# Kernel tuning notes

Hardware: AMD Instinct MI355X
Metric: run time of the kernel (lower is better)

## Reference

```python
import jax, jax.numpy as jnp
import numpy as np

BN_EPS = 1e-5


def setup_inputs() -> dict:
    key = jax.random.key(0)
    ks = jax.random.split(key, 8)
    B, C, N = 4, 256, 4096
    s = 1.0 / np.sqrt(C)
    return {
        "feature": jax.random.normal(ks[0], (B, C, N, 1), dtype=jnp.float32),
        "Wa": jax.random.normal(ks[1], (C, C), dtype=jnp.float32) * s,
        "ba": jnp.zeros((C,), dtype=jnp.float32),
        "Wb": jax.random.normal(ks[2], (C, C), dtype=jnp.float32) * s,
        "bb": jnp.zeros((C,), dtype=jnp.float32),
        "Wm": jax.random.normal(ks[3], (C, C), dtype=jnp.float32) * s,
        "bm": jnp.zeros((C,), dtype=jnp.float32),
        "gamma": jnp.ones((C,), dtype=jnp.float32),
        "beta": jnp.zeros((C,), dtype=jnp.float32),
        "rmean": jnp.zeros((C,), dtype=jnp.float32),
        "rvar": jnp.ones((C,), dtype=jnp.float32),
        "alpha": jnp.zeros((1,), dtype=jnp.float32),
    }


def reference(feature, Wa, ba, Wb, bb, Wm, bm, gamma, beta, rmean, rvar, alpha):
    # feature: [B, C, N, 1]; 1x1 convs are per-point linear maps over channels.
    x = feature[..., 0]  # [B, C, N]
    a = jnp.einsum('oc,bcn->bon', Wa, x) + ba[None, :, None]  # fc_a
    b = jnp.einsum('oc,bcn->bon', Wb, x) + bb[None, :, None]  # fc_b
    # att = softmax(a^T @ b) over last dim: [B, N, N]
    att = jax.nn.softmax(jnp.einsum('bcn,bcm->bnm', a, b), axis=2)
    # mlp: 1x1 conv + eval-mode BatchNorm
    m = jnp.einsum('oc,bcn->bon', Wm, x) + bm[None, :, None]
    inv = jax.lax.rsqrt(rvar + BN_EPS)
    m = (m - rmean[None, :, None]) * (inv * gamma)[None, :, None] + beta[None, :, None]
    # f = att @ m^T -> [B, N, C], back to [B, C, N]
    f = jnp.einsum('bnm,bcm->bcn', att, m)
    return feature + alpha[0] * f[..., None]
```

## Files before the change

### kernel.cpp

```cpp
#include <hip/hip_runtime.h>
#include <hip/hip_bf16.h>

typedef __bf16 bf16x8 __attribute__((ext_vector_type(8)));
typedef float f32x4 __attribute__((ext_vector_type(4)));
typedef float f32x16 __attribute__((ext_vector_type(16)));
typedef int i32x2 __attribute__((ext_vector_type(2)));
typedef int i32x4 __attribute__((ext_vector_type(4)));
typedef int i32x8 __attribute__((ext_vector_type(8)));
typedef unsigned int u32;

#define MFMA16 __builtin_amdgcn_mfma_f32_16x16x32_bf16
#define MFMASC(a, b, c) \
  __builtin_amdgcn_mfma_scale_f32_32x32x64_f8f6f4((a), (b), (c), 0, 0, 0, 0x7F7F7F7F, 0, 0x7F7F7F7F)

#define LOG2E 1.44269504f

__device__ __forceinline__ unsigned short f2b(float f) {
  return __builtin_bit_cast(unsigned short, (__bf16)f);
}

__device__ __forceinline__ u32 pk4(float a, float b, float c, float d) {
  int v = __builtin_amdgcn_cvt_pk_fp8_f32(a, b, 0, false);
  v = __builtin_amdgcn_cvt_pk_fp8_f32(c, d, v, true);
  return (u32)v;
}

__device__ __forceinline__ void gload_lds16(const void* g, void* l) {
  __builtin_amdgcn_global_load_lds(
      (const __attribute__((address_space(1))) unsigned int*)g,
      (__attribute__((address_space(3))) unsigned int*)l, 16, 0, 0);
}

__global__ __launch_bounds__(256) void k_wconv(const float* __restrict__ Wa,
                                               const float* __restrict__ Wb,
                                               const float* __restrict__ Wm,
                                               unsigned short* __restrict__ W16) {
  const int m = blockIdx.y;
  const float* W = (m == 0) ? Wa : (m == 1) ? Wb : Wm;
  const int i = (blockIdx.x * 256 + threadIdx.x) * 8;
  float4 a = *reinterpret_cast<const float4*>(W + i);
  float4 b = *reinterpret_cast<const float4*>(W + i + 4);
  ushort4 lo, hi;
  lo.x = f2b(a.x); lo.y = f2b(a.y); lo.z = f2b(a.z); lo.w = f2b(a.w);
  hi.x = f2b(b.x); hi.y = f2b(b.y); hi.z = f2b(b.z); hi.w = f2b(b.w);
  unsigned short* dst = W16 + m * 65536 + i;
  *reinterpret_cast<ushort4*>(dst) = lo;
  *reinterpret_cast<ushort4*>(dst + 4) = hi;
}

__global__ __launch_bounds__(256) void k_proj(
    const float* __restrict__ x, const unsigned short* __restrict__ W16,
    const float* __restrict__ ba, const float* __restrict__ bb,
    const float* __restrict__ bm, const float* __restrict__ gamma,
    const float* __restrict__ beta, const float* __restrict__ rmean,
    const float* __restrict__ rvar,
    unsigned char* __restrict__ Q8, unsigned char* __restrict__ K8,
    unsigned char* __restrict__ V8) {
  __shared__ float tile[256][33];
  __shared__ __align__(16) unsigned short XT_lds[32 * 256];
  const int nt = blockIdx.x, b = blockIdx.y;
  const int n0 = nt * 32;
  const int tid = threadIdx.x, w = tid >> 6, l = tid & 63;
  const int li = l & 15, lk = l >> 4;
  {
    const int cr = tid >> 3, j4 = (tid & 7) * 4;
#pragma unroll
    for (int p = 0; p < 8; ++p) {
      int c = p * 32 + cr;
      float4 v = *reinterpret_cast<const float4*>(
          x + ((size_t)(b * 256 + c)) * 4096 + n0 + j4);
      tile[c][j4] = v.x; tile[c][j4 + 1] = v.y;
      tile[c][j4 + 2] = v.z; tile[c][j4 + 3] = v.w;
    }
  }
  __syncthreads();
  {
    const int n = tid & 31, cb8 = (tid >> 5) * 32;
#pragma unroll
    for (int p = 0; p < 8; ++p) {
      int c0 = cb8 + p * 4;
      ushort4 o;
      o.x = f2b(tile[c0][n]); o.y = f2b(tile[c0 + 1][n]);
      o.z = f2b(tile[c0 + 2][n]); o.w = f2b(tile[c0 + 3][n]);
      unsigned off = ((unsigned)(n * 512 + c0 * 2)) ^ (unsigned)((n & 7) << 4);
      *reinterpret_cast<ushort4*>((char*)XT_lds + off) = o;
    }
  }
  __syncthreads();
  bf16x8 af[2][8];
#pragma unroll
  for (int rs = 0; rs < 2; ++rs) {
    const int row = rs * 16 + li;
#pragma unroll
    for (int kk = 0; kk < 8; ++kk) {
      unsigned off = ((unsigned)(row * 512 + kk * 64 + lk * 16)) ^ (unsigned)((row & 7) << 4);
      af[rs][kk] = *reinterpret_cast<const bf16x8*>((const char*)XT_lds + off);
    }
  }
  const int ofb = w * 4;
  f32x4 zero = {0.f, 0.f, 0.f, 0.f};
  f32x4 acc[2][4];
  {
#pragma unroll
    for (int rs = 0; rs < 2; ++rs)
#pragma unroll
      for (int i = 0; i < 4; ++i) acc[rs][i] = zero;
#pragma unroll
    for (int kk = 0; kk < 8; ++kk)
#pragma unroll
      for (int of = 0; of < 4; ++of) {
        bf16x8 bfv = *reinterpret_cast<const bf16x8*>(
            W16 + (size_t)((ofb + of) * 16 + li) * 256 + kk * 32 + lk * 8);
        acc[0][of] = MFMA16(bfv, af[0][kk], acc[0][of], 0, 0, 0);
        acc[1][of] = MFMA16(bfv, af[1][kk], acc[1][of], 0, 0, 0);
      }
#pragma unroll
    for (int rs = 0; rs < 2; ++rs) {
      const int n = n0 + rs * 16 + li;
      unsigned char* out = Q8 + ((size_t)b * 4096 + n) * 256;
#pragma unroll
      for (int of = 0; of < 4; ++of) {
        int c0 = (ofb + of) * 16 + lk * 4;
        float4 bs = *reinterpret_cast<const float4*>(ba + c0);
        u32 v = pk4((acc[rs][of][0] + bs.x) * LOG2E, (acc[rs][of][1] + bs.y) * LOG2E,
                    (acc[rs][of][2] + bs.z) * LOG2E, (acc[rs][of][3] + bs.w) * LOG2E);
        *reinterpret_cast<u32*>(out + c0) = v;
      }
    }
  }
  {
#pragma unroll
    for (int rs = 0; rs < 2; ++rs)
#pragma unroll
      for (int i = 0; i < 4; ++i) acc[rs][i] = zero;
#pragma unroll
    for (int kk = 0; kk < 8; ++kk)
#pragma unroll
      for (int of = 0; of < 4; ++of) {
        bf16x8 bfv = *reinterpret_cast<const bf16x8*>(
            W16 + 65536 + (size_t)((ofb + of) * 16 + li) * 256 + kk * 32 + lk * 8);
        acc[0][of] = MFMA16(bfv, af[0][kk], acc[0][of], 0, 0, 0);
        acc[1][of] = MFMA16(bfv, af[1][kk], acc[1][of], 0, 0, 0);
      }
#pragma unroll
    for (int rs = 0; rs < 2; ++rs) {
      const int n = n0 + rs * 16 + li;
      unsigned char* out = K8 + ((size_t)b * 4096 + n) * 256;
#pragma unroll
      for (int of = 0; of < 4; ++of) {
        int c0 = (ofb + of) * 16 + lk * 4;
        float4 bs = *reinterpret_cast<const float4*>(bb + c0);
        u32 v = pk4(acc[rs][of][0] + bs.x, acc[rs][of][1] + bs.y,
                    acc[rs][of][2] + bs.z, acc[rs][of][3] + bs.w);
        *reinterpret_cast<u32*>(out + c0) = v;
      }
    }
  }
  {
#pragma unroll
    for (int rs = 0; rs < 2; ++rs)
#pragma unroll
      for (int i = 0; i < 4; ++i) acc[rs][i] = zero;
#pragma unroll
    for (int kk = 0; kk < 8; ++kk)
#pragma unroll
      for (int of = 0; of < 4; ++of) {
        bf16x8 bfv = *reinterpret_cast<const bf16x8*>(
            W16 + 131072 + (size_t)((ofb + of) * 16 + li) * 256 + kk * 32 + lk * 8);
        acc[0][of] = MFMA16(af[0][kk], bfv, acc[0][of], 0, 0, 0);
        acc[1][of] = MFMA16(af[1][kk], bfv, acc[1][of], 0, 0, 0);
      }
#pragma unroll
    for (int of = 0; of < 4; ++of) {
      int c = (ofb + of) * 16 + li;
      float g = rsqrtf(rvar[c] + 1e-5f) * gamma[c];
      float sh = (bm[c] - rmean[c]) * g + beta[c];
#pragma unroll
      for (int rs = 0; rs < 2; ++rs) {
        const int nn0 = n0 + rs * 16 + lk * 4;
        u32 v = pk4(acc[rs][of][0] * g + sh, acc[rs][of][1] * g + sh,
                    acc[rs][of][2] * g + sh, acc[rs][of][3] * g + sh);
        *reinterpret_cast<u32*>(V8 + (((size_t)b * 512 + (nn0 >> 3)) * 256 + c) * 8 + (nn0 & 7)) = v;
      }
    }
  }
}

__global__ __launch_bounds__(256, 2) void k_attn(
    const unsigned char* __restrict__ Q8, const unsigned char* __restrict__ K8,
    const unsigned char* __restrict__ V8, unsigned short* __restrict__ part,
    float* __restrict__ mpart, float* __restrict__ lpart) {
  __shared__ __align__(16) unsigned char K_lds[2][64 * 256];
  __shared__ __align__(16) unsigned char V_lds[2][8 * 2048];
  const int bid = blockIdx.x;
  const int swz = (bid & 7) * 64 + (bid >> 3);
  const int qt = swz & 31;
  const int bs = swz >> 5;
  const int b = bs >> 2, s = bs & 3;
  const int tid = threadIdx.x, w = tid >> 6, l = tid & 63;
  const int q = l & 31, hi = l >> 5;
  const int rowq = qt * 128 + w * 32 + q;
  i32x8 qf8[4];
  const unsigned char* qp = Q8 + ((size_t)b * 4096 + rowq) * 256 + hi * 32;
#pragma unroll
  for (int kk = 0; kk < 4; ++kk) {
    i32x4 lo = *reinterpret_cast<const i32x4*>(qp + kk * 64);
    i32x4 hh = *reinterpret_cast<const i32x4*>(qp + kk * 64 + 16);
    qf8[kk] = (i32x8){lo[0], lo[1], lo[2], lo[3], hh[0], hh[1], hh[2], hh[3]};
  }
  f32x16 acc[8];
#pragma unroll
  for (int i = 0; i < 8; ++i)
#pragma unroll
    for (int r = 0; r < 16; ++r) acc[i][r] = 0.f;
  float mr = -3e38f, lr = 0.f;

  auto stageK = [&](int buf, int k0) {
#pragma unroll
    for (int g = 0; g < 4; ++g) {
      int row = w * 16 + g * 4 + (l >> 4);
      int c16 = (l & 15) ^ ((row & 7) << 1);
      const unsigned char* src = K8 + ((size_t)b * 4096 + k0 + row) * 256 + c16 * 16;
      gload_lds16(src, &K_lds[buf][(w * 16 + g * 4) * 256]);
    }
  };
  auto stageV = [&](int buf, int k0) {
    const size_t k8b = (size_t)b * 512 + (k0 >> 3);
#pragma unroll
    for (int g = 0; g < 4; ++g) {
      int slab = w * 2 + (g >> 1);
      int pos = (g & 1) * 64 + l;
      const unsigned char* src = V8 + (k8b + slab) * 2048 + pos * 16;
      gload_lds16(src, &V_lds[buf][slab * 2048 + (g & 1) * 1024]);
    }
  };

  const int kbase = s * 1024;
  stageK(0, kbase);
  stageV(0, kbase);
  asm volatile("s_waitcnt vmcnt(0)" ::: "memory");
  __syncthreads();
  int cur = 0;
  for (int t = 0; t < 16; ++t) {
    if (t < 15) { stageK(cur ^ 1, kbase + (t + 1) * 64); stageV(cur ^ 1, kbase + (t + 1) * 64); }
    f32x16 S0, S1;
#pragma unroll
    for (int r = 0; r < 16; ++r) { S0[r] = 0.f; S1[r] = 0.f; }
    __builtin_amdgcn_s_setprio(1);
#pragma unroll
    for (int kk = 0; kk < 4; ++kk) {
      int off = ((kk * 2 + hi) ^ (q & 7)) << 5;
      const unsigned char* kr0 = &K_lds[cur][q * 256 + off];
      const unsigned char* kr1 = &K_lds[cur][(32 + q) * 256 + off];
      i32x4 a0 = *reinterpret_cast<const i32x4*>(kr0);
      i32x4 a1 = *reinterpret_cast<const i32x4*>(kr0 + 16);
      i32x4 b0 = *reinterpret_cast<const i32x4*>(kr1);
      i32x4 b1 = *reinterpret_cast<const i32x4*>(kr1 + 16);
      i32x8 kf0 = (i32x8){a0[0], a0[1], a0[2], a0[3], a1[0], a1[1], a1[2], a1[3]};
      i32x8 kf1 = (i32x8){b0[0], b0[1], b0[2], b0[3], b1[0], b1[1], b1[2], b1[3]};
      S0 = MFMASC(kf0, qf8[kk], S0);
      S1 = MFMASC(kf1, qf8[kk], S1);
    }
    __builtin_amdgcn_s_setprio(0);
    float pmax = fmaxf(S0[0], S1[0]);
#pragma unroll
    for (int r = 1; r < 16; ++r) pmax = fmaxf(pmax, fmaxf(S0[r], S1[r]));
    pmax = fmaxf(pmax, __shfl_xor(pmax, 32));
    if (!__all(pmax - mr <= 7.0f)) {
      float nm = fmaxf(mr, pmax);
      float sc = exp2f(mr - nm);
      mr = nm;
      lr *= sc;
#pragma unroll
      for (int cb = 0; cb < 8; ++cb)
#pragma unroll
        for (int r = 0; r < 16; ++r) acc[cb][r] *= sc;
    }
    float p0[16], p1[16];
    float sum = 0.f;
#pragma unroll
    for (int r = 0; r < 16; ++r) { p0[r] = exp2f(S0[r] - mr); sum += p0[r]; }
#pragma unroll
    for (int r = 0; r < 16; ++r) { p1[r] = exp2f(S1[r] - mr); sum += p1[r]; }
    sum += __shfl_xor(sum, 32);
    lr += sum;
    u32 A0 = pk4(p0[0], p0[1], p0[2], p0[3]);
    u32 A1 = pk4(p0[4], p0[5], p0[6], p0[7]);
    u32 A2 = pk4(p0[8], p0[9], p0[10], p0[11]);
    u32 A3 = pk4(p0[12], p0[13], p0[14], p0[15]);
    u32 B0 = pk4(p1[0], p1[1], p1[2], p1[3]);
    u32 B1 = pk4(p1[4], p1[5], p1[6], p1[7]);
    u32 B2 = pk4(p1[8], p1[9], p1[10], p1[11]);
    u32 B3 = pk4(p1[12], p1[13], p1[14], p1[15]);
    asm volatile("v_permlane32_swap_b32 %0, %1" : "+v"(A0), "+v"(B0));
    asm volatile("v_permlane32_swap_b32 %0, %1" : "+v"(A1), "+v"(B1));
    asm volatile("v_permlane32_swap_b32 %0, %1" : "+v"(A2), "+v"(B2));
    asm volatile("v_permlane32_swap_b32 %0, %1" : "+v"(A3), "+v"(B3));
    i32x8 pb = (i32x8){(int)A0, (int)B0, (int)A1, (int)B1,
                       (int)A2, (int)B2, (int)A3, (int)B3};
    __builtin_amdgcn_s_setprio(1);
#pragma unroll
    for (int cb = 0; cb < 8; ++cb) {
      const unsigned char* vb = &V_lds[cur][(hi * 4) * 2048 + (cb * 32 + q) * 8];
      i32x2 v0 = *reinterpret_cast<const i32x2*>(vb);
      i32x2 v1 = *reinterpret_cast<const i32x2*>(vb + 2048);
      i32x2 v2 = *reinterpret_cast<const i32x2*>(vb + 4096);
      i32x2 v3 = *reinterpret_cast<const i32x2*>(vb + 6144);
      i32x8 vf = (i32x8){v0[0], v0[1], v1[0], v1[1], v2[0], v2[1], v3[0], v3[1]};
      acc[cb] = MFMASC(vf, pb, acc[cb]);
    }
    __builtin_amdgcn_s_setprio(0);
    asm volatile("s_waitcnt vmcnt(0)" ::: "memory");
    __syncthreads();
    cur ^= 1;
  }
  const int sb = s * 4 + b;
  size_t pbase = ((size_t)sb * 4096 + rowq) * 256;
#pragma unroll
  for (int cb = 0; cb < 8; ++cb)
#pragma unroll
    for (int g = 0; g < 4; ++g) {
      ushort4 o;
      o.x = f2b(acc[cb][g * 4 + 0]); o.y = f2b(acc[cb][g * 4 + 1]);
      o.z = f2b(acc[cb][g * 4 + 2]); o.w = f2b(acc[cb][g * 4 + 3]);
      *reinterpret_cast<ushort4*>(&part[pbase + cb * 32 + g * 8 + hi * 4]) = o;
    }
  if (hi == 0) {
    mpart[sb * 4096 + rowq] = mr;
    lpart[sb * 4096 + rowq] = lr;
  }
}

__global__ __launch_bounds__(256) void k_comb(
    const unsigned short* __restrict__ part, const float* __restrict__ mpart,
    const float* __restrict__ lpart, const float* __restrict__ feat,
    const float* __restrict__ alpha, float* __restrict__ out) {
  __shared__ float wgt[4][64];
  __shared__ float tile[64][261];
  const int nt = blockIdx.x, b = blockIdx.y;
  const int n0 = nt * 64;
  const int tid = threadIdx.x;
  if (tid < 64) {
    int qn = n0 + tid;
    float m[4], lv[4];
#pragma unroll
    for (int s = 0; s < 4; ++s) {
      m[s] = mpart[(s * 4 + b) * 4096 + qn];
      lv[s] = lpart[(s * 4 + b) * 4096 + qn];
    }
    float M = fmaxf(fmaxf(m[0], m[1]), fmaxf(m[2], m[3]));
    float e[4], L = 0.f;
#pragma unroll
    for (int s = 0; s < 4; ++s) { e[s] = exp2f(m[s] - M); L += e[s] * lv[s]; }
    float inv = 1.0f / L;
#pragma unroll
    for (int s = 0; s < 4; ++s) wgt[s][tid] = e[s] * inv;
  }
  __syncthreads();
  const int row = tid >> 2;
  const int c0 = (tid & 3) * 64;
  float acc[64];
#pragma unroll
  for (int k = 0; k < 64; ++k) acc[k] = 0.f;
  for (int s = 0; s < 4; ++s) {
    float ww = wgt[s][row];
    const unsigned short* p = part + (((size_t)(s * 4 + b)) * 4096 + n0 + row) * 256 + c0;
#pragma unroll
    for (int ch = 0; ch < 8; ++ch) {
      bf16x8 v = *reinterpret_cast<const bf16x8*>(p + ch * 8);
#pragma unroll
      for (int j = 0; j < 8; ++j) acc[ch * 8 + j] += ww * (float)v[j];
    }
  }
#pragma unroll
  for (int k = 0; k < 64; ++k) tile[row][c0 + k] = acc[k];
  __syncthreads();
  const float av = alpha[0];
  const int j = tid & 15, cb = tid >> 4;
#pragma unroll
  for (int p = 0; p < 16; ++p) {
    int c = cb * 16 + p;
    size_t gbase = ((size_t)(b * 256 + c)) * 4096 + n0 + j * 4;
    float4 f4 = *reinterpret_cast<const float4*>(feat + gbase);
    float4 o;
    o.x = f4.x + av * tile[j * 4 + 0][c];
    o.y = f4.y + av * tile[j * 4 + 1][c];
    o.z = f4.z + av * tile[j * 4 + 2][c];
    o.w = f4.w + av * tile[j * 4 + 3][c];
    *reinterpret_cast<float4*>(out + gbase) = o;
  }
}

extern "C" void kernel_launch(void* const* d_in, const int* in_sizes, int n_in,
                              void* d_out, int out_size, void* d_ws, size_t ws_size,
                              hipStream_t stream) {
  const float* feat  = (const float*)d_in[0];
  const float* Wa    = (const float*)d_in[1];
  const float* ba    = (const float*)d_in[2];
  const float* Wb    = (const float*)d_in[3];
  const float* bb    = (const float*)d_in[4];
  const float* Wm    = (const float*)d_in[5];
  const float* bm    = (const float*)d_in[6];
  const float* gamma = (const float*)d_in[7];
  const float* beta  = (const float*)d_in[8];
  const float* rmean = (const float*)d_in[9];
  const float* rvar  = (const float*)d_in[10];
  const float* alpha = (const float*)d_in[11];
  float* out = (float*)d_out;
  char* ws = (char*)d_ws;
  unsigned char*  Q8   = (unsigned char*)(ws);
  unsigned char*  K8   = (unsigned char*)(ws + ((size_t)4 << 20));
  unsigned char*  V8   = (unsigned char*)(ws + ((size_t)8 << 20));
  unsigned short* part = (unsigned short*)(ws + ((size_t)16 << 20));
  unsigned short* W16  = (unsigned short*)(ws + ((size_t)48 << 20));
  float* mpart = (float*)(ws + ((size_t)48 << 20) + 393216);
  float* lpart = (float*)(ws + ((size_t)48 << 20) + 393216 + 262144);

  k_wconv<<<dim3(32, 3), 256, 0, stream>>>(Wa, Wb, Wm, W16);
  k_proj<<<dim3(128, 4), 256, 0, stream>>>(feat, W16, ba, bb, bm, gamma, beta,
                                           rmean, rvar, Q8, K8, V8);
  k_attn<<<dim3(512), 256, 0, stream>>>(Q8, K8, V8, part, mpart, lpart);
  k_comb<<<dim3(64, 4), 256, 0, stream>>>(part, mpart, lpart, feat, alpha, out);
}
```

Baseline: 121.2 us.

## Re-layout V8 into 32-key chunks for wide LDS reads and unroll attn loop

Changes the V8 global layout from 8-key slabs to 32-key chunks per channel so each lane reads a contiguous 32-byte fragment from LDS instead of four 8-byte pieces. K fragment reads also become single 32-byte loads. Staging pointers are precomputed and the double-buffered loop is unrolled by two so buffer indices are compile-time constants. The max and sum reductions become trees, and the projection tile store becomes one float4 with padding changed to 36. Padding 36 may add bank conflicts in the transposed column reads, and 32-byte V reads with a 32-byte row stride could conflict in LDS.

```diff
diff --git a/kernel.cpp b/kernel.cpp
--- a/kernel.cpp
+++ b/kernel.cpp
@@ -4,7 +4,6 @@
 typedef __bf16 bf16x8 __attribute__((ext_vector_type(8)));
 typedef float f32x4 __attribute__((ext_vector_type(4)));
 typedef float f32x16 __attribute__((ext_vector_type(16)));
-typedef int i32x2 __attribute__((ext_vector_type(2)));
 typedef int i32x4 __attribute__((ext_vector_type(4)));
 typedef int i32x8 __attribute__((ext_vector_type(8)));
 typedef unsigned int u32;
@@ -56,7 +55,7 @@
     const float* __restrict__ rvar,
     unsigned char* __restrict__ Q8, unsigned char* __restrict__ K8,
     unsigned char* __restrict__ V8) {
-  __shared__ float tile[256][33];
+  __shared__ float tile[256][36];
   __shared__ __align__(16) unsigned short XT_lds[32 * 256];
   const int nt = blockIdx.x, b = blockIdx.y;
   const int n0 = nt * 32;
@@ -69,8 +68,7 @@
       int c = p * 32 + cr;
       float4 v = *reinterpret_cast<const float4*>(
           x + ((size_t)(b * 256 + c)) * 4096 + n0 + j4);
-      tile[c][j4] = v.x; tile[c][j4 + 1] = v.y;
-      tile[c][j4 + 2] = v.z; tile[c][j4 + 3] = v.w;
+      *reinterpret_cast<float4*>(&tile[c][j4]) = v;
     }
   }
   __syncthreads();
@@ -180,7 +178,8 @@
         const int nn0 = n0 + rs * 16 + lk * 4;
         u32 v = pk4(acc[rs][of][0] * g + sh, acc[rs][of][1] * g + sh,
                     acc[rs][of][2] * g + sh, acc[rs][of][3] * g + sh);
-        *reinterpret_cast<u32*>(V8 + (((size_t)b * 512 + (nn0 >> 3)) * 256 + c) * 8 + (nn0 & 7)) = v;
+        *reinterpret_cast<u32*>(
+            V8 + ((size_t)b * 128 + (nn0 >> 5)) * 8192 + c * 32 + (nn0 & 31)) = v;
       }
     }
   }
@@ -190,8 +189,8 @@
     const unsigned char* __restrict__ Q8, const unsigned char* __restrict__ K8,
     const unsigned char* __restrict__ V8, unsigned short* __restrict__ part,
     float* __restrict__ mpart, float* __restrict__ lpart) {
-  __shared__ __align__(16) unsigned char K_lds[2][64 * 256];
-  __shared__ __align__(16) unsigned char V_lds[2][8 * 2048];
+  __shared__ __align__(32) unsigned char K_lds[2][64 * 256];
+  __shared__ __align__(32) unsigned char V_lds[2][2 * 8192];
   const int bid = blockIdx.x;
   const int swz = (bid & 7) * 64 + (bid >> 3);
   const int qt = swz & 31;
@@ -215,57 +214,51 @@
     for (int r = 0; r < 16; ++r) acc[i][r] = 0.f;
   float mr = -3e38f, lr = 0.f;
 
-  auto stageK = [&](int buf, int k0) {
-#pragma unroll
-    for (int g = 0; g < 4; ++g) {
-      int row = w * 16 + g * 4 + (l >> 4);
-      int c16 = (l & 15) ^ ((row & 7) << 1);
-      const unsigned char* src = K8 + ((size_t)b * 4096 + k0 + row) * 256 + c16 * 16;
-      gload_lds16(src, &K_lds[buf][(w * 16 + g * 4) * 256]);
-    }
+  const int kbase = s * 1024;
+  const unsigned char* kp[4];
+  const unsigned char* vp[4];
+#pragma unroll
+  for (int g = 0; g < 4; ++g) {
+    int row = w * 16 + g * 4 + (l >> 4);
+    int c16 = (l & 15) ^ ((row & 7) << 1);
+    kp[g] = K8 + ((size_t)b * 4096 + kbase + row) * 256 + c16 * 16;
+    int chunk = g * 4 + w;
+    vp[g] = V8 + ((size_t)b * 128 + (kbase >> 5)) * 8192 + chunk * 1024 + l * 16;
+  }
+  auto stageK = [&](int buf, int t) {
+#pragma unroll
+    for (int g = 0; g < 4; ++g)
+      gload_lds16(kp[g] + t * 16384, &K_lds[buf][(w * 16 + g * 4) * 256]);
   };
-  auto stageV = [&](int buf, int k0) {
-    const size_t k8b = (size_t)b * 512 + (k0 >> 3);
-#pragma unroll
-    for (int g = 0; g < 4; ++g) {
-      int slab = w * 2 + (g >> 1);
-      int pos = (g & 1) * 64 + l;
-      const unsigned char* src = V8 + (k8b + slab) * 2048 + pos * 16;
-      gload_lds16(src, &V_lds[buf][slab * 2048 + (g & 1) * 1024]);
-    }
+  auto stageV = [&](int buf, int t) {
+#pragma unroll
+    for (int g = 0; g < 4; ++g)
+      gload_lds16(vp[g] + t * 16384, &V_lds[buf][(g * 4 + w) * 1024]);
   };
 
-  const int kbase = s * 1024;
-  stageK(0, kbase);
-  stageV(0, kbase);
-  asm volatile("s_waitcnt vmcnt(0)" ::: "memory");
-  __syncthreads();
-  int cur = 0;
-  for (int t = 0; t < 16; ++t) {
-    if (t < 15) { stageK(cur ^ 1, kbase + (t + 1) * 64); stageV(cur ^ 1, kbase + (t + 1) * 64); }
+  auto body = [&](int cur, int t) {
+    if (t + 1 < 16) { stageK(cur ^ 1, t + 1); stageV(cur ^ 1, t + 1); }
     f32x16 S0, S1;
 #pragma unroll
     for (int r = 0; r < 16; ++r) { S0[r] = 0.f; S1[r] = 0.f; }
     __builtin_amdgcn_s_setprio(1);
 #pragma unroll
     for (int kk = 0; kk < 4; ++kk) {
-      int off = ((kk * 2 + hi) ^ (q & 7)) << 5;
-      const unsigned char* kr0 = &K_lds[cur][q * 256 + off];
-      const unsigned char* kr1 = &K_lds[cur][(32 + q) * 256 + off];
-      i32x4 a0 = *reinterpret_cast<const i32x4*>(kr0);
-      i32x4 a1 = *reinterpret_cast<const i32x4*>(kr0 + 16);
-      i32x4 b0 = *reinterpret_cast<const i32x4*>(kr1);
-      i32x4 b1 = *reinterpret_cast<const i32x4*>(kr1 + 16);
-      i32x8 kf0 = (i32x8){a0[0], a0[1], a0[2], a0[3], a1[0], a1[1], a1[2], a1[3]};
-      i32x8 kf1 = (i32x8){b0[0], b0[1], b0[2], b0[3], b1[0], b1[1], b1[2], b1[3]};
+      int off = (((kk * 2 + hi) ^ (q & 7)) << 5);
+      i32x8 kf0 = *reinterpret_cast<const i32x8*>(&K_lds[cur][q * 256 + off]);
+      i32x8 kf1 = *reinterpret_cast<const i32x8*>(&K_lds[cur][(32 + q) * 256 + off]);
       S0 = MFMASC(kf0, qf8[kk], S0);
       S1 = MFMASC(kf1, qf8[kk], S1);
     }
     __builtin_amdgcn_s_setprio(0);
-    float pmax = fmaxf(S0[0], S1[0]);
-#pragma unroll
-    for (int r = 1; r < 16; ++r) pmax = fmaxf(pmax, fmaxf(S0[r], S1[r]));
-    pmax = fmaxf(pmax, __shfl_xor(pmax, 32));
+    float tm[16];
+#pragma unroll
+    for (int r = 0; r < 16; ++r) tm[r] = fmaxf(S0[r], S1[r]);
+#pragma unroll
+    for (int d = 8; d >= 1; d >>= 1)
+#pragma unroll
+      for (int r = 0; r < d; ++r) tm[r] = fmaxf(tm[r], tm[r + d]);
+    float pmax = fmaxf(tm[0], __shfl_xor(tm[0], 32));
     if (!__all(pmax - mr <= 7.0f)) {
       float nm = fmaxf(mr, pmax);
       float sc = exp2f(mr - nm);
@@ -276,22 +269,24 @@
 #pragma unroll
         for (int r = 0; r < 16; ++r) acc[cb][r] *= sc;
     }
-    float p0[16], p1[16];
-    float sum = 0.f;
-#pragma unroll
-    for (int r = 0; r < 16; ++r) { p0[r] = exp2f(S0[r] - mr); sum += p0[r]; }
-#pragma unroll
-    for (int r = 0; r < 16; ++r) { p1[r] = exp2f(S1[r] - mr); sum += p1[r]; }
-    sum += __shfl_xor(sum, 32);
-    lr += sum;
-    u32 A0 = pk4(p0[0], p0[1], p0[2], p0[3]);
-    u32 A1 = pk4(p0[4], p0[5], p0[6], p0[7]);
-    u32 A2 = pk4(p0[8], p0[9], p0[10], p0[11]);
-    u32 A3 = pk4(p0[12], p0[13], p0[14], p0[15]);
-    u32 B0 = pk4(p1[0], p1[1], p1[2], p1[3]);
-    u32 B1 = pk4(p1[4], p1[5], p1[6], p1[7]);
-    u32 B2 = pk4(p1[8], p1[9], p1[10], p1[11]);
-    u32 B3 = pk4(p1[12], p1[13], p1[14], p1[15]);
+#pragma unroll
+    for (int r = 0; r < 16; ++r) { S0[r] = exp2f(S0[r] - mr); S1[r] = exp2f(S1[r] - mr); }
+    float ts[16];
+#pragma unroll
+    for (int r = 0; r < 16; ++r) ts[r] = S0[r] + S1[r];
+#pragma unroll
+    for (int d = 8; d >= 1; d >>= 1)
+#pragma unroll
+      for (int r = 0; r < d; ++r) ts[r] += ts[r + d];
+    lr += ts[0] + __shfl_xor(ts[0], 32);
+    u32 A0 = pk4(S0[0], S0[1], S0[2], S0[3]);
+    u32 A1 = pk4(S0[4], S0[5], S0[6], S0[7]);
+    u32 A2 = pk4(S0[8], S0[9], S0[10], S0[11]);
+    u32 A3 = pk4(S0[12], S0[13], S0[14], S0[15]);
+    u32 B0 = pk4(S1[0], S1[1], S1[2], S1[3]);
+    u32 B1 = pk4(S1[4], S1[5], S1[6], S1[7]);
+    u32 B2 = pk4(S1[8], S1[9], S1[10], S1[11]);
+    u32 B3 = pk4(S1[12], S1[13], S1[14], S1[15]);
     asm volatile("v_permlane32_swap_b32 %0, %1" : "+v"(A0), "+v"(B0));
     asm volatile("v_permlane32_swap_b32 %0, %1" : "+v"(A1), "+v"(B1));
     asm volatile("v_permlane32_swap_b32 %0, %1" : "+v"(A2), "+v"(B2));
@@ -301,18 +296,22 @@
     __builtin_amdgcn_s_setprio(1);
 #pragma unroll
     for (int cb = 0; cb < 8; ++cb) {
-      const unsigned char* vb = &V_lds[cur][(hi * 4) * 2048 + (cb * 32 + q) * 8];
-      i32x2 v0 = *reinterpret_cast<const i32x2*>(vb);
-      i32x2 v1 = *reinterpret_cast<const i32x2*>(vb + 2048);
-      i32x2 v2 = *reinterpret_cast<const i32x2*>(vb + 4096);
-      i32x2 v3 = *reinterpret_cast<const i32x2*>(vb + 6144);
-      i32x8 vf = (i32x8){v0[0], v0[1], v1[0], v1[1], v2[0], v2[1], v3[0], v3[1]};
+      i32x8 vf = *reinterpret_cast<const i32x8*>(
+          &V_lds[cur][hi * 8192 + (cb * 32 + q) * 32]);
       acc[cb] = MFMASC(vf, pb, acc[cb]);
     }
     __builtin_amdgcn_s_setprio(0);
     asm volatile("s_waitcnt vmcnt(0)" ::: "memory");
     __syncthreads();
-    cur ^= 1;
+  };
+
+  stageK(0, 0);
+  stageV(0, 0);
+  asm volatile("s_waitcnt vmcnt(0)" ::: "memory");
+  __syncthreads();
+  for (int t = 0; t < 16; t += 2) {
+    body(0, t);
+    body(1, t + 1);
   }
   const int sb = s * 4 + b;
   size_t pbase = ((size_t)sb * 4096 + rowq) * 256;
```

Measured after the change: 130.6 us. 1.08x slower.
